# Performance work log

Hardware: AMD Instinct MI355X
Metric: run time of the kernel (lower is better)

## Reference

```python
import jax, jax.numpy as jnp
import numpy as np

U, B, I, D, L = 50000, 20000, 100000, 64, 2
E_UB, E_UI, E_BI = 800000, 1000000, 800000
E_BIAGG, E_UIAGG = 800000, 1000000
UPS_UB = UPS_UI = UPS_BI = 0.1
XI = jnp.array([1.0 / 3, 1.0 / 3, 1.0 / 3], dtype=jnp.float32)  # layer coefs (len L+1)
OMEGA, G1, G2, TAU, LAM1, LAM2 = 0.5, 0.5, 0.5, 0.25, 0.04, 1e-5
BATCH = 2048


def l2norm(x, axis=-1):
    n = jnp.linalg.norm(x, axis=axis, keepdims=True)
    return x / jnp.maximum(n, 1e-12)


def spmm(rows, cols, vals, x, n):
    # sparse [n, m] @ dense [m, D] via gather + segment-sum over COO entries
    return jax.ops.segment_sum(vals[:, None] * x[cols], rows, num_segments=n)


def graph_propagate(rows, cols, vals, A, Bf, noise, ups, xi):
    n = A.shape[0] + Bf.shape[0]
    feats = jnp.concatenate([A, Bf], axis=0)
    alls = [feats]
    for l in range(L):
        feats = spmm(rows, cols, vals, feats, n)
        feats = feats + jnp.sign(feats) * l2norm(noise[l]) * ups  # noise injection
        alls.append(l2norm(feats, axis=1))
    out = jnp.sum(jnp.stack(alls, axis=1) * xi[None, :, None], axis=1)  # weighted layer sum [n, D]
    return out[: A.shape[0]], out[A.shape[0] :]


def graph_aggregate(rows, cols, vals, x, noise, ups, n):
    agg = spmm(rows, cols, vals, x, n)
    return agg + jnp.sign(agg) * l2norm(noise) * ups


def cl_loss(pos, aug):
    pos = l2norm(pos, 1)
    aug = l2norm(aug, 1)
    pos_score = jnp.exp(jnp.sum(pos * aug, axis=1) / TAU)
    ttl = jnp.sum(jnp.exp(pos @ aug.T / TAU), axis=1)
    return -jnp.mean(jnp.log(pos_score / ttl))


def dcbr_forward(users_feature, bundles_feature, items_feature,
                 ub_rows, ub_cols, ub_vals, ui_rows, ui_cols, ui_vals,
                 bi_rows, bi_cols, bi_vals, biagg_rows, biagg_cols, biagg_vals,
                 uiagg_rows, uiagg_cols, uiagg_vals,
                 noise_UB, noise_UI, noise_BI, noise_agg_BI, noise_agg_UI,
                 users, bundles):
    UB_u, UB_b = graph_propagate(ub_rows, ub_cols, ub_vals, users_feature, bundles_feature, noise_UB, UPS_UB, XI)
    UI_u, UI_i = graph_propagate(ui_rows, ui_cols, ui_vals, users_feature, items_feature, noise_UI, UPS_UI, XI)
    UI_b = graph_aggregate(biagg_rows, biagg_cols, biagg_vals, UI_i, noise_agg_BI, UPS_BI, B)
    BI_b, BI_i = graph_propagate(bi_rows, bi_cols, bi_vals, bundles_feature, items_feature, noise_BI, UPS_BI, XI)
    BI_u = graph_aggregate(uiagg_rows, uiagg_cols, uiagg_vals, BI_i, noise_agg_UI, UPS_UI, U)
    users_rep = OMEGA * UI_u + (1 - OMEGA) * BI_u
    bundles_rep = OMEGA * UI_b + (1 - OMEGA) * BI_b
    u_emb = users_rep[users]          # [batch, 1, D] -> broadcasts over negatives
    b_emb = bundles_rep[bundles]      # [batch, 2, D]
    pred = jnp.sum(u_emb * b_emb, axis=2)  # [batch, 2]
    pos, neg = pred[:, :1], pred[:, 1:]
    reg = jnp.sum(users_feature ** 2) + jnp.sum(bundles_feature ** 2) + jnp.sum(items_feature ** 2)
    bpr = -jnp.mean(jax.nn.log_sigmoid(pos - neg)) + LAM2 * reg
    u0, b0 = users[:, 0], bundles[:, 0]
    ub_u, ui_us, bi_us = UB_u[u0], UI_u[u0], BI_u[u0]
    ub_bb, ui_bb, bi_bb = UB_b[b0], UI_b[b0], BI_b[b0]
    u_inter = cl_loss(ub_u, ui_us) + cl_loss(ub_u, bi_us) + cl_loss(ui_us, bi_us)
    b_inter = cl_loss(ub_bb, ui_bb) + cl_loss(ub_bb, bi_bb) + cl_loss(ui_bb, bi_bb)
    u_intra = cl_loss(ub_u, ub_u) + cl_loss(ui_us, ui_us) + cl_loss(bi_us, bi_us)
    b_intra = cl_loss(ub_bb, ub_bb) + cl_loss(ui_bb, ui_bb) + cl_loss(bi_bb, bi_bb)
    cl = LAM1 * (G1 * (u_inter + b_inter) + G2 * (u_intra + b_intra))
    return bpr, cl


def setup_inputs():
    key = jax.random.key(0)
    k = jax.random.split(key, 16)

    def prop_edges(kk, nA, nB, e):
        k1, k2, k3 = jax.random.split(kk, 3)
        a = jax.random.randint(k1, (e,), 0, nA, dtype=jnp.int32)
        b = jax.random.randint(k2, (e,), 0, nB, dtype=jnp.int32) + nA
        v = jax.random.uniform(k3, (e,), jnp.float32, 0.01, 0.2)  # degree-normalized weights
        return jnp.concatenate([a, b]), jnp.concatenate([b, a]), jnp.concatenate([v, v])

    def agg_edges(kk, nA, nB, e):
        k1, k2, k3 = jax.random.split(kk, 3)
        return (jax.random.randint(k1, (e,), 0, nA, dtype=jnp.int32),
                jax.random.randint(k2, (e,), 0, nB, dtype=jnp.int32),
                jax.random.uniform(k3, (e,), jnp.float32, 0.01, 0.2))

    ub_rows, ub_cols, ub_vals = prop_edges(k[0], U, B, E_UB)
    ui_rows, ui_cols, ui_vals = prop_edges(k[1], U, I, E_UI)
    bi_rows, bi_cols, bi_vals = prop_edges(k[2], B, I, E_BI)
    biagg_rows, biagg_cols, biagg_vals = agg_edges(k[3], B, I, E_BIAGG)
    uiagg_rows, uiagg_cols, uiagg_vals = agg_edges(k[4], U, I, E_UIAGG)
    s = 0.02  # xavier-normal-ish scale
    return {
        'users_feature': jax.random.normal(k[5], (U, D), jnp.float32) * s,
        'bundles_feature': jax.random.normal(k[6], (B, D), jnp.float32) * s,
        'items_feature': jax.random.normal(k[7], (I, D), jnp.float32) * s,
        'ub_rows': ub_rows, 'ub_cols': ub_cols, 'ub_vals': ub_vals,
        'ui_rows': ui_rows, 'ui_cols': ui_cols, 'ui_vals': ui_vals,
        'bi_rows': bi_rows, 'bi_cols': bi_cols, 'bi_vals': bi_vals,
        'biagg_rows': biagg_rows, 'biagg_cols': biagg_cols, 'biagg_vals': biagg_vals,
        'uiagg_rows': uiagg_rows, 'uiagg_cols': uiagg_cols, 'uiagg_vals': uiagg_vals,
        'noise_UB': jax.random.uniform(k[8], (L, U + B, D), jnp.float32),
        'noise_UI': jax.random.uniform(k[9], (L, U + I, D), jnp.float32),
        'noise_BI': jax.random.uniform(k[10], (L, B + I, D), jnp.float32),
        'noise_agg_BI': jax.random.uniform(k[11], (B, D), jnp.float32),
        'noise_agg_UI': jax.random.uniform(k[12], (U, D), jnp.float32),
        'users': jax.random.randint(k[13], (BATCH, 1), 0, U, dtype=jnp.int32),
        'bundles': jax.random.randint(k[14], (BATCH, 2), 0, B, dtype=jnp.int32),
    }


def reference(users_feature, bundles_feature, items_feature,
              ub_rows, ub_cols, ub_vals, ui_rows, ui_cols, ui_vals,
              bi_rows, bi_cols, bi_vals, biagg_rows, biagg_cols, biagg_vals,
              uiagg_rows, uiagg_cols, uiagg_vals,
              noise_UB, noise_UI, noise_BI, noise_agg_BI, noise_agg_UI,
              users, bundles):
    return dcbr_forward(users_feature, bundles_feature, items_feature,
                        ub_rows, ub_cols, ub_vals, ui_rows, ui_cols, ui_vals,
                        bi_rows, bi_cols, bi_vals, biagg_rows, biagg_cols, biagg_vals,
                        uiagg_rows, uiagg_cols, uiagg_vals,
                        noise_UB, noise_UI, noise_BI, noise_agg_BI, noise_agg_UI,
                        users, bundles)
```

## Files before the change

kernel.cpp:

```cpp
#include <hip/hip_runtime.h>
#include <cmath>
#include <climits>

#define DD 64

namespace {

constexpr int U_N = 50000, B_N = 20000, I_N = 100000;
constexpr int BATCH = 2048;

constexpr int N1 = 340000, N2 = 70000;
constexpr int SHIFT1 = 10, SHIFT2 = 8;
constexpr int NB1 = (N1 + (1 << SHIFT1) - 1) >> SHIFT1;
constexpr int NB2 = (N2 + (1 << SHIFT2) - 1) >> SHIFT2;

typedef __attribute__((ext_vector_type(8))) short short8;
typedef __attribute__((ext_vector_type(4))) float floatx4;

__device__ __forceinline__ float wave_sum(float v) {
#pragma unroll
  for (int off = 32; off > 0; off >>= 1) v += __shfl_xor(v, off);
  return v;
}

__device__ __forceinline__ unsigned short f2bf(float f) {
  unsigned u = __float_as_uint(f);
  unsigned r = (u + 0x7FFFu + ((u >> 16) & 1u)) >> 16;
  return (unsigned short)r;
}

__device__ __forceinline__ float sgn(float x) {
  return (x > 0.f) ? 1.f : ((x < 0.f) ? -1.f : 0.f);
}

__global__ void k_tobf16(const float* __restrict__ x, unsigned short* __restrict__ o, int n4) {
  int i = blockIdx.x * 256 + threadIdx.x;
  if (i >= n4) return;
  float4 v = ((const float4*)x)[i];
  uint2 p;
  p.x = (unsigned)f2bf(v.x) | ((unsigned)f2bf(v.y) << 16);
  p.y = (unsigned)f2bf(v.z) | ((unsigned)f2bf(v.w) << 16);
  ((uint2*)o)[i] = p;
}

__global__ __launch_bounds__(512) void k_bhist(const int* __restrict__ rows, int nnz,
                                               int row_off, int shift,
                                               const unsigned char* __restrict__ flags,
                                               int* __restrict__ bcnt) {
  __shared__ int h[512];
  int t = threadIdx.x;
  h[t] = 0;
  __syncthreads();
  int tile0 = blockIdx.x * 8192;
#pragma unroll
  for (int i = 0; i < 16; ++i) {
    int e = tile0 + i * 512 + t;
    if (e < nnz) {
      int r = rows[e] + row_off;
      if (!flags || flags[r]) atomicAdd(&h[r >> shift], 1);
    }
  }
  __syncthreads();
  if (h[t]) atomicAdd(&bcnt[t], h[t]);
}

__global__ void k_bucket_scan(const int* __restrict__ bcnt, int nb, int* __restrict__ bbase,
                              int* __restrict__ bcur, int* __restrict__ rowptr_end) {
  int t = threadIdx.x;
  int lane = t & 63, w = t >> 6;
  int v = (t < nb) ? bcnt[t] : 0;
  int inc = v;
#pragma unroll
  for (int off = 1; off < 64; off <<= 1) {
    int y = __shfl_up(inc, off);
    if (lane >= off) inc += y;
  }
  __shared__ int wsum[8];
  if (lane == 63) wsum[w] = inc;
  __syncthreads();
  int wadd = 0;
  for (int i = 0; i < w; ++i) wadd += wsum[i];
  inc += wadd;
  if (t < nb) { bbase[t] = inc - v; bcur[t] = inc - v; }
  if (t == 511) { bbase[nb] = inc; *rowptr_end = inc; }
}

__global__ __launch_bounds__(512) void k_binscatter(const int* __restrict__ rows,
                                                    const int* __restrict__ cols,
                                                    const float* __restrict__ vals, int nnz,
                                                    int row_off, int shift,
                                                    int nAth, int offA, int offB,
                                                    const unsigned char* __restrict__ flags,
                                                    int* __restrict__ bcur,
                                                    int2* __restrict__ ebin_cv) {
  __shared__ int cnt[512];
  __shared__ int gbase[512];
  int t = threadIdx.x;
  int tile0 = blockIdx.x * 8192;
  cnt[t] = 0;
  __syncthreads();
  int r[16], rank[16];
#pragma unroll
  for (int i = 0; i < 16; ++i) {
    int e = tile0 + i * 512 + t;
    rank[i] = -1;
    if (e < nnz) {
      r[i] = rows[e] + row_off;
      if (!flags || flags[r[i]]) rank[i] = atomicAdd(&cnt[r[i] >> shift], 1);
    }
  }
  __syncthreads();
  int c = cnt[t];
  if (c > 0) gbase[t] = atomicAdd(&bcur[t], c);
  __syncthreads();
  int mask = (1 << shift) - 1;
#pragma unroll
  for (int i = 0; i < 16; ++i) {
    int e = tile0 + i * 512 + t;
    if (rank[i] >= 0) {
      int pos = gbase[r[i] >> shift] + rank[i];
      int col = cols[e];
      int gcol = (col < nAth) ? col + offA : col + offB;
      ebin_cv[pos] = make_int2(((r[i] & mask) << 20) | gcol, __float_as_int(vals[e]));
    }
  }
}

__global__ __launch_bounds__(1024) void k_place(const int* __restrict__ bbase, int shift,
                                                int nrows, const int2* __restrict__ ebin_cv,
                                                int* __restrict__ rowptr,
                                                int2* __restrict__ epack) {
  int b = blockIdx.x;
  int bsize = 1 << shift;
  int row0 = b << shift;
  int t = threadIdx.x;
  __shared__ int rcnt[1024];
  __shared__ int wsum[16];
  int ebase = bbase[b], eend = bbase[b + 1];
  if (t < bsize) rcnt[t] = 0;
  __syncthreads();
  for (int e = ebase + t; e < eend; e += 1024)
    atomicAdd(&rcnt[ebin_cv[e].x >> 20], 1);
  __syncthreads();
  int v = (t < bsize) ? rcnt[t] : 0;
  int inc = v;
  int lane = t & 63, w = t >> 6;
#pragma unroll
  for (int off = 1; off < 64; off <<= 1) {
    int y = __shfl_up(inc, off);
    if (lane >= off) inc += y;
  }
  if (lane == 63) wsum[w] = inc;
  __syncthreads();
  int wadd = 0;
  for (int i = 0; i < w; ++i) wadd += wsum[i];
  inc += wadd;
  int excl = inc - v;
  int nr = nrows - row0;
  if (nr > bsize) nr = bsize;
  if (t < nr) rowptr[row0 + t] = ebase + excl;
  __syncthreads();
  if (t < bsize) rcnt[t] = excl;
  __syncthreads();
  for (int e = ebase + t; e < eend; e += 1024) {
    int2 cv = ebin_cv[e];
    int pos = ebase + atomicAdd(&rcnt[cv.x >> 20], 1);
    epack[pos] = make_int2(cv.x & 0xFFFFF, cv.y);
  }
}

__global__ void k_spmm1(const int* __restrict__ rowptr, const int2* __restrict__ epack,
                        const uint2* __restrict__ xg, const float* __restrict__ noise,
                        uint2* __restrict__ s2g, int n, int nAth, int offA, int offB) {
  long long t = (long long)blockIdx.x * 256 + threadIdx.x;
  int row = (int)(t >> 6), lane = (int)(t & 63);
  if (row >= n) return;
  int q = lane >> 4, c = lane & 15;
  int s = rowptr[row], e = rowptr[row + 1];
  float4 a[4];
#pragma unroll
  for (int j = 0; j < 4; ++j) a[j] = (float4){0.f, 0.f, 0.f, 0.f};
  for (int kk = s; kk < e; kk += 16) {
#pragma unroll
    for (int j = 0; j < 4; ++j) {
      int i = kk + 4 * j + q;
      int2 ed = (i < e) ? epack[i] : make_int2(0, 0);
      uint2 d = xg[ed.x * 16 + c];
      float v = __int_as_float(ed.y);
      a[j].x = fmaf(v, __uint_as_float(d.x << 16), a[j].x);
      a[j].y = fmaf(v, __uint_as_float(d.x & 0xffff0000u), a[j].y);
      a[j].z = fmaf(v, __uint_as_float(d.y << 16), a[j].z);
      a[j].w = fmaf(v, __uint_as_float(d.y & 0xffff0000u), a[j].w);
    }
  }
  float4 g;
  g.x = a[0].x + a[1].x + a[2].x + a[3].x;
  g.y = a[0].y + a[1].y + a[2].y + a[3].y;
  g.z = a[0].z + a[1].z + a[2].z + a[3].z;
  g.w = a[0].w + a[1].w + a[2].w + a[3].w;
  g.x += __shfl_xor(g.x, 16); g.y += __shfl_xor(g.y, 16);
  g.z += __shfl_xor(g.z, 16); g.w += __shfl_xor(g.w, 16);
  g.x += __shfl_xor(g.x, 32); g.y += __shfl_xor(g.y, 32);
  g.z += __shfl_xor(g.z, 32); g.w += __shfl_xor(g.w, 32);
  float4 nz = ((const float4*)(noise + (size_t)row * DD))[c];
  float nn = wave_sum(nz.x * nz.x + nz.y * nz.y + nz.z * nz.z + nz.w * nz.w) * 0.25f;
  float nf = 0.1f / fmaxf(sqrtf(nn), 1e-12f);
  if (lane < 16) {
    float4 fv;
    fv.x = g.x + sgn(g.x) * nz.x * nf;
    fv.y = g.y + sgn(g.y) * nz.y * nf;
    fv.z = g.z + sgn(g.z) * nz.z * nf;
    fv.w = g.w + sgn(g.w) * nz.w * nf;
    uint2 o;
    o.x = (unsigned)f2bf(fv.x) | ((unsigned)f2bf(fv.y) << 16);
    o.y = (unsigned)f2bf(fv.z) | ((unsigned)f2bf(fv.w) << 16);
    int grow = (row < nAth) ? row + offA : row + offB;
    s2g[grow * 16 + c] = o;
  }
}

__global__ void k_spmm2(const int* __restrict__ rowptr, const int2* __restrict__ epack,
                        const uint2* __restrict__ s2g, const uint2* __restrict__ xg,
                        const float* __restrict__ noise, float* __restrict__ outp,
                        int n, int nAth, int offA, int offB) {
  long long t = (long long)blockIdx.x * 256 + threadIdx.x;
  int row = (int)(t >> 6), lane = (int)(t & 63);
  if (row >= n) return;
  int q = lane >> 4, c = lane & 15;
  int s = rowptr[row], e = rowptr[row + 1];
  float4 a[4];
#pragma unroll
  for (int j = 0; j < 4; ++j) a[j] = (float4){0.f, 0.f, 0.f, 0.f};
  for (int kk = s; kk < e; kk += 16) {
#pragma unroll
    for (int j = 0; j < 4; ++j) {
      int i = kk + 4 * j + q;
      int2 ed = (i < e) ? epack[i] : make_int2(0, 0);
      uint2 d = s2g[ed.x * 16 + c];
      float v = __int_as_float(ed.y);
      a[j].x = fmaf(v, __uint_as_float(d.x << 16), a[j].x);
      a[j].y = fmaf(v, __uint_as_float(d.x & 0xffff0000u), a[j].y);
      a[j].z = fmaf(v, __uint_as_float(d.y << 16), a[j].z);
      a[j].w = fmaf(v, __uint_as_float(d.y & 0xffff0000u), a[j].w);
    }
  }
  float4 g;
  g.x = a[0].x + a[1].x + a[2].x + a[3].x;
  g.y = a[0].y + a[1].y + a[2].y + a[3].y;
  g.z = a[0].z + a[1].z + a[2].z + a[3].z;
  g.w = a[0].w + a[1].w + a[2].w + a[3].w;
  g.x += __shfl_xor(g.x, 16); g.y += __shfl_xor(g.y, 16);
  g.z += __shfl_xor(g.z, 16); g.w += __shfl_xor(g.w, 16);
  g.x += __shfl_xor(g.x, 32); g.y += __shfl_xor(g.y, 32);
  g.z += __shfl_xor(g.z, 32); g.w += __shfl_xor(g.w, 32);
  float4 nz = ((const float4*)(noise + (size_t)row * DD))[c];
  float nn = wave_sum(nz.x * nz.x + nz.y * nz.y + nz.z * nz.z + nz.w * nz.w) * 0.25f;
  float nf = 0.1f / fmaxf(sqrtf(nn), 1e-12f);
  float4 fv;
  fv.x = g.x + sgn(g.x) * nz.x * nf;
  fv.y = g.y + sgn(g.y) * nz.y * nf;
  fv.z = g.z + sgn(g.z) * nz.z * nf;
  fv.w = g.w + sgn(g.w) * nz.w * nf;
  float fn2 = wave_sum(fv.x * fv.x + fv.y * fv.y + fv.z * fv.z + fv.w * fv.w) * 0.25f;
  float inv2 = (1.f / 3.f) / fmaxf(sqrtf(fn2), 1e-12f);
  int grow = (row < nAth) ? row + offA : row + offB;
  uint2 s1p = s2g[grow * 16 + c];
  float4 s1;
  s1.x = __uint_as_float(s1p.x << 16);
  s1.y = __uint_as_float(s1p.x & 0xffff0000u);
  s1.z = __uint_as_float(s1p.y << 16);
  s1.w = __uint_as_float(s1p.y & 0xffff0000u);
  float fn1 = wave_sum(s1.x * s1.x + s1.y * s1.y + s1.z * s1.z + s1.w * s1.w) * 0.25f;
  float inv1 = (1.f / 3.f) / fmaxf(sqrtf(fn1), 1e-12f);
  uint2 x0p = xg[grow * 16 + c];
  float4 x0;
  x0.x = __uint_as_float(x0p.x << 16);
  x0.y = __uint_as_float(x0p.x & 0xffff0000u);
  x0.z = __uint_as_float(x0p.y << 16);
  x0.w = __uint_as_float(x0p.y & 0xffff0000u);
  if (lane < 16) {
    float4 o;
    o.x = x0.x * (1.f / 3.f) + s1.x * inv1 + fv.x * inv2;
    o.y = x0.y * (1.f / 3.f) + s1.y * inv1 + fv.y * inv2;
    o.z = x0.z * (1.f / 3.f) + s1.z * inv1 + fv.z * inv2;
    o.w = x0.w * (1.f / 3.f) + s1.w * inv1 + fv.w * inv2;
    ((float4*)(outp + (size_t)row * DD))[c] = o;
  }
}

__global__ void k_agg_s(const int* __restrict__ rowptr, const int2* __restrict__ epack,
                        const float* __restrict__ x, const float* __restrict__ noise,
                        const int* __restrict__ ids, int nids, float* __restrict__ out) {
  long long t = (long long)blockIdx.x * 256 + threadIdx.x;
  int w = (int)(t >> 6), lane = (int)(t & 63);
  if (w >= nids) return;
  int row = ids[w];
  int q = lane >> 4, c = lane & 15;
  int s = rowptr[row], e = rowptr[row + 1];
  float4 a0 = {0.f, 0.f, 0.f, 0.f}, a1 = {0.f, 0.f, 0.f, 0.f};
  for (int kk = s; kk < e; kk += 8) {
    int i0 = kk + q, i1 = kk + 4 + q;
    int2 e0 = (i0 < e) ? epack[i0] : make_int2(0, 0);
    int2 e1 = (i1 < e) ? epack[i1] : make_int2(0, 0);
    float4 x0 = ((const float4*)(x + (size_t)e0.x * DD))[c];
    float4 x1 = ((const float4*)(x + (size_t)e1.x * DD))[c];
    float v0 = __int_as_float(e0.y), v1 = __int_as_float(e1.y);
    a0.x = fmaf(v0, x0.x, a0.x); a0.y = fmaf(v0, x0.y, a0.y);
    a0.z = fmaf(v0, x0.z, a0.z); a0.w = fmaf(v0, x0.w, a0.w);
    a1.x = fmaf(v1, x1.x, a1.x); a1.y = fmaf(v1, x1.y, a1.y);
    a1.z = fmaf(v1, x1.z, a1.z); a1.w = fmaf(v1, x1.w, a1.w);
  }
  float4 g;
  g.x = a0.x + a1.x; g.y = a0.y + a1.y; g.z = a0.z + a1.z; g.w = a0.w + a1.w;
  g.x += __shfl_xor(g.x, 16); g.y += __shfl_xor(g.y, 16);
  g.z += __shfl_xor(g.z, 16); g.w += __shfl_xor(g.w, 16);
  g.x += __shfl_xor(g.x, 32); g.y += __shfl_xor(g.y, 32);
  g.z += __shfl_xor(g.z, 32); g.w += __shfl_xor(g.w, 32);
  float4 nz = ((const float4*)(noise + (size_t)row * DD))[c];
  float nn = wave_sum(nz.x * nz.x + nz.y * nz.y + nz.z * nz.z + nz.w * nz.w) * 0.25f;
  float nf = 0.1f / fmaxf(sqrtf(nn), 1e-12f);
  if (lane < 16) {
    float4 fv;
    fv.x = g.x + sgn(g.x) * nz.x * nf;
    fv.y = g.y + sgn(g.y) * nz.y * nf;
    fv.z = g.z + sgn(g.z) * nz.z * nf;
    fv.w = g.w + sgn(g.w) * nz.w * nf;
    ((float4*)(out + (size_t)w * DD))[c] = fv;
  }
}

__global__ void k_flag(const int* __restrict__ users, const int* __restrict__ bundles,
                       unsigned char* __restrict__ flags) {
  int t = blockIdx.x * 256 + threadIdx.x;
  if (t < BATCH) flags[20000 + users[t]] = 1;
  if (t < 2 * BATCH) flags[bundles[t]] = 1;
}


__global__ void k_bpr(const float* __restrict__ o_UI, const float* __restrict__ biuS,
                      const float* __restrict__ uibS, const float* __restrict__ o_BI,
                      const int* __restrict__ users, const int* __restrict__ bundles,
                      float* __restrict__ bpr_terms) {
  long long t = (long long)blockIdx.x * 256 + threadIdx.x;
  int w = (int)(t >> 6);
  int lane = (int)(t & 63);
  if (w >= BATCH) return;
  int u = users[w];
  int b0 = bundles[2 * w], b1 = bundles[2 * w + 1];
  float ur = 0.5f * (o_UI[(size_t)u * DD + lane] + biuS[(size_t)w * DD + lane]);
  float br0 = 0.5f * (uibS[(size_t)(2 * w) * DD + lane] + o_BI[(size_t)b0 * DD + lane]);
  float br1 = 0.5f * (uibS[(size_t)(2 * w + 1) * DD + lane] + o_BI[(size_t)b1 * DD + lane]);
  float pos = wave_sum(ur * br0);
  float neg = wave_sum(ur * br1);
  if (lane == 0) {
    float x = pos - neg;
    float loss = (x > 0.f) ? log1pf(expf(-x)) : (-x + log1pf(expf(x)));
    bpr_terms[w] = loss;
  }
}

__global__ void k_sumsq_p(const float* __restrict__ x, int n4, float* __restrict__ partials) {
  float s = 0.f;
  for (int i = blockIdx.x * 256 + threadIdx.x; i < n4; i += gridDim.x * 256) {
    float4 v = ((const float4*)x)[i];
    s += v.x * v.x + v.y * v.y + v.z * v.z + v.w * v.w;
  }
  s = wave_sum(s);
  __shared__ float part[4];
  if ((threadIdx.x & 63) == 0) part[threadIdx.x >> 6] = s;
  __syncthreads();
  if (threadIdx.x == 0) partials[blockIdx.x] = part[0] + part[1] + part[2] + part[3];
}

__global__ void k_gather(const float* __restrict__ o_UB, const float* __restrict__ o_UI,
                         const float* __restrict__ o_BI, const float* __restrict__ uibS,
                         const float* __restrict__ biuS, const int* __restrict__ users,
                         const int* __restrict__ bundles, float* __restrict__ P,
                         unsigned short* __restrict__ Pb) {
  long long t = (long long)blockIdx.x * 256 + threadIdx.x;
  int w = (int)(t >> 6);
  int lane = (int)(t & 63);
  if (w >= 6 * BATCH) return;
  int k = w / BATCH, b = w % BATCH;
  const float* src;
  if (k == 0)      src = o_UB + (size_t)users[b] * DD;
  else if (k == 1) src = o_UI + (size_t)users[b] * DD;
  else if (k == 2) src = biuS + (size_t)b * DD;
  else if (k == 3) src = o_UB + (size_t)(U_N + bundles[2 * b]) * DD;
  else if (k == 4) src = uibS + (size_t)(2 * b) * DD;
  else             src = o_BI + (size_t)bundles[2 * b] * DD;
  float v = src[lane];
  float n2 = wave_sum(v * v);
  float inv = 1.f / fmaxf(sqrtf(n2), 1e-12f);
  float pv = v * inv;
  P[(size_t)w * DD + lane] = pv;
  Pb[(size_t)w * DD + lane] = f2bf(pv);
}

__global__ void k_clpair_mfma(const unsigned short* __restrict__ Pb,
                              float* __restrict__ ttl) {
  const int pairX[12] = {0, 0, 1, 0, 1, 2, 3, 3, 4, 3, 4, 5};
  const int pairY[12] = {1, 2, 2, 0, 1, 2, 4, 5, 5, 3, 4, 5};
  int wid = threadIdx.x >> 6;
  int lane = threadIdx.x & 63;
  int wtile = blockIdx.x * 4 + wid;
  int p = wtile >> 8;
  int rest = wtile & 255;
  int it = rest >> 3, jc = rest & 7;
  const unsigned short* X = Pb + (size_t)pairX[p] * BATCH * DD;
  const unsigned short* Y = Pb + (size_t)pairY[p] * BATCH * DD;
  int r = lane & 15, q = lane >> 4;
  short8 A[2][4];
#pragma unroll
  for (int kh = 0; kh < 2; ++kh)
#pragma unroll
    for (int ii = 0; ii < 4; ++ii)
      A[kh][ii] = *(const short8*)(X + (size_t)(it * 64 + ii * 16 + r) * DD + kh * 32 + q * 8);
  float rs[4][4];
#pragma unroll
  for (int ii = 0; ii < 4; ++ii)
#pragma unroll
    for (int g = 0; g < 4; ++g) rs[ii][g] = 0.f;
  for (int jn = 0; jn < 4; ++jn) {
    int j0 = jc * 256 + jn * 64;
    floatx4 acc[4][4];
#pragma unroll
    for (int ii = 0; ii < 4; ++ii)
#pragma unroll
      for (int jj = 0; jj < 4; ++jj) acc[ii][jj] = (floatx4){0.f, 0.f, 0.f, 0.f};
#pragma unroll
    for (int kh = 0; kh < 2; ++kh) {
      short8 Bf[4];
#pragma unroll
      for (int jj = 0; jj < 4; ++jj)
        Bf[jj] = *(const short8*)(Y + (size_t)(j0 + jj * 16 + r) * DD + kh * 32 + q * 8);
#pragma unroll
      for (int ii = 0; ii < 4; ++ii)
#pragma unroll
        for (int jj = 0; jj < 4; ++jj)
          acc[ii][jj] = __builtin_amdgcn_mfma_f32_16x16x32_bf16(A[kh][ii], Bf[jj],
                                                                acc[ii][jj], 0, 0, 0);
    }
#pragma unroll
    for (int ii = 0; ii < 4; ++ii)
#pragma unroll
      for (int jj = 0; jj < 4; ++jj)
#pragma unroll
        for (int g = 0; g < 4; ++g) rs[ii][g] += __expf(4.0f * acc[ii][jj][g]);
  }
#pragma unroll
  for (int off = 1; off < 16; off <<= 1)
#pragma unroll
    for (int ii = 0; ii < 4; ++ii)
#pragma unroll
      for (int g = 0; g < 4; ++g) rs[ii][g] += __shfl_xor(rs[ii][g], off);
  if (r == 0) {
#pragma unroll
    for (int ii = 0; ii < 4; ++ii)
#pragma unroll
      for (int g = 0; g < 4; ++g)
        unsafeAtomicAdd(&ttl[(size_t)p * BATCH + it * 64 + ii * 16 + q * 4 + g],
                        rs[ii][g]);
  }
}

__global__ void k_cldiag(const float* __restrict__ P, float* __restrict__ ttl) {
  const int pairX[12] = {0, 0, 1, 0, 1, 2, 3, 3, 4, 3, 4, 5};
  const int pairY[12] = {1, 2, 2, 0, 1, 2, 4, 5, 5, 3, 4, 5};
  long long t = (long long)blockIdx.x * 256 + threadIdx.x;
  int w = (int)(t >> 6);
  int lane = (int)(t & 63);
  if (w >= 12 * BATCH) return;
  int p = w / BATCH, i = w % BATCH;
  float xv = P[((size_t)pairX[p] * BATCH + i) * DD + lane];
  float yv = P[((size_t)pairY[p] * BATCH + i) * DD + lane];
  float d = wave_sum(xv * yv);
  if (lane == 0) ttl[(size_t)p * BATCH + i] = logf(ttl[(size_t)p * BATCH + i]) - d * 4.0f;
}

__global__ void k_finalred(const float* __restrict__ bpr_terms,
                           const float* __restrict__ cl_terms,
                           const float* __restrict__ partials,
                           float* __restrict__ out) {
  int t = threadIdx.x;
  float bpr = 0.f, reg = 0.f, inter = 0.f, intra = 0.f;
  for (int i = t; i < BATCH; i += 1024) bpr += bpr_terms[i];
  for (int i = t; i < 768; i += 1024) reg += partials[i];
  for (int i = t; i < 12 * BATCH; i += 1024) {
    int p = i >> 11;
    float v = cl_terms[i];
    if ((p % 6) < 3) inter += v; else intra += v;
  }
  bpr = wave_sum(bpr); reg = wave_sum(reg);
  inter = wave_sum(inter); intra = wave_sum(intra);
  __shared__ float sb[16], sr[16], si[16], sx[16];
  int w = t >> 6, lane = t & 63;
  if (lane == 0) { sb[w] = bpr; sr[w] = reg; si[w] = inter; sx[w] = intra; }
  __syncthreads();
  if (t == 0) {
    float Bs = 0, Rs = 0, Is = 0, Xs = 0;
    for (int i = 0; i < 16; ++i) { Bs += sb[i]; Rs += sr[i]; Is += si[i]; Xs += sx[i]; }
    out[0] = Bs / (float)BATCH + 1e-5f * Rs;
    out[1] = 0.04f * (0.5f * Is + 0.5f * Xs) / (float)BATCH;
  }
}

}

extern "C" void kernel_launch(void* const* d_in, const int* in_sizes, int n_in,
                              void* d_out, int out_size, void* d_ws, size_t ws_size,
                              hipStream_t stream) {
  const float* usersF = (const float*)d_in[0];
  const float* bundlesF = (const float*)d_in[1];
  const float* itemsF = (const float*)d_in[2];
  const int* ub_rows = (const int*)d_in[3];
  const int* ub_cols = (const int*)d_in[4];
  const float* ub_vals = (const float*)d_in[5];
  const int* ui_rows = (const int*)d_in[6];
  const int* ui_cols = (const int*)d_in[7];
  const float* ui_vals = (const float*)d_in[8];
  const int* bi_rows = (const int*)d_in[9];
  const int* bi_cols = (const int*)d_in[10];
  const float* bi_vals = (const float*)d_in[11];
  const int* biagg_rows = (const int*)d_in[12];
  const int* biagg_cols = (const int*)d_in[13];
  const float* biagg_vals = (const float*)d_in[14];
  const int* uiagg_rows = (const int*)d_in[15];
  const int* uiagg_cols = (const int*)d_in[16];
  const float* uiagg_vals = (const float*)d_in[17];
  const float* noise_UB = (const float*)d_in[18];
  const float* noise_UI = (const float*)d_in[19];
  const float* noise_BI = (const float*)d_in[20];
  const float* noise_agg_BI = (const float*)d_in[21];
  const float* noise_agg_UI = (const float*)d_in[22];
  const int* users = (const int*)d_in[23];
  const int* bundles = (const int*)d_in[24];
  int nnz_ub = in_sizes[3], nnz_ui = in_sizes[6], nnz_bi = in_sizes[9];
  int nnz_biagg = in_sizes[12], nnz_uiagg = in_sizes[15];

  float* ws = (float*)d_ws;
  size_t off = 0;
  float* o_UB = ws + off; off += (size_t)(U_N + B_N) * DD;
  float* o_UI = ws + off; off += (size_t)(U_N + I_N) * DD;
  float* o_BI = ws + off; off += (size_t)(B_N + I_N) * DD;
  float* uibS = ws + off; off += (size_t)2 * BATCH * DD;
  float* biuS = ws + off; off += (size_t)BATCH * DD;
  unsigned short* s2g16 = (unsigned short*)(ws + off); off += (size_t)170000 * DD / 2;
  unsigned short* xb16  = (unsigned short*)(ws + off); off += (size_t)170000 * DD / 2;
  float* P    = ws + off; off += (size_t)6 * BATCH * DD;
  float* ttl  = ws + off; off += (size_t)12 * BATCH;
  float* bprT = ws + off; off += BATCH;
  float* prt  = ws + off; off += 768;
  int* rptr  = (int*)(ws + off); off += N1 + 1;
  int* bcnt  = (int*)(ws + off); off += 512;
  int* bbase = (int*)(ws + off); off += 520;
  int* bcur  = (int*)(ws + off); off += 512;
  unsigned char* flags = (unsigned char*)(ws + off); off += 17500;
  off = (off + 1) & ~(size_t)1;
  int2* epack = (int2*)(ws + off); off += (size_t)5200000 * 2;
  if (ws_size < off * sizeof(float)) return;

  unsigned short* Pb = (unsigned short*)s2g16;
  int2* ebin_cv1 = (int2*)ws;
  int2* ebin_cv2 = (int2*)s2g16;

  const uint2* xgv = (const uint2*)xb16;
  uint2* s2gv = (uint2*)s2g16;

  auto gb = [](int nnz) { return (nnz + 8191) / 8192; };

  k_tobf16<<<(U_N * 16 + 255) / 256, 256, 0, stream>>>(usersF, xb16, U_N * 16);
  k_tobf16<<<(B_N * 16 + 255) / 256, 256, 0, stream>>>(bundlesF, xb16 + (size_t)U_N * DD,
                                                       B_N * 16);
  k_tobf16<<<(I_N * 16 + 255) / 256, 256, 0, stream>>>(itemsF, xb16 + (size_t)(U_N + B_N) * DD,
                                                       I_N * 16);

  int* rp_ub = rptr, * rp_ui = rptr + 70000, * rp_bi = rptr + 220000;
  hipMemsetAsync(bcnt, 0, 512 * sizeof(int), stream);
  k_bhist<<<gb(nnz_ub), 512, 0, stream>>>(ub_rows, nnz_ub, 0, SHIFT1, nullptr, bcnt);
  k_bhist<<<gb(nnz_ui), 512, 0, stream>>>(ui_rows, nnz_ui, 70000, SHIFT1, nullptr, bcnt);
  k_bhist<<<gb(nnz_bi), 512, 0, stream>>>(bi_rows, nnz_bi, 220000, SHIFT1, nullptr, bcnt);
  k_bucket_scan<<<1, 512, 0, stream>>>(bcnt, NB1, bbase, bcur, rptr + N1);
  k_binscatter<<<gb(nnz_ub), 512, 0, stream>>>(ub_rows, ub_cols, ub_vals, nnz_ub, 0, SHIFT1,
                                               INT_MAX, 0, 0, nullptr, bcur, ebin_cv1);
  k_binscatter<<<gb(nnz_ui), 512, 0, stream>>>(ui_rows, ui_cols, ui_vals, nnz_ui, 70000, SHIFT1,
                                               50000, 0, 20000, nullptr, bcur, ebin_cv1);
  k_binscatter<<<gb(nnz_bi), 512, 0, stream>>>(bi_rows, bi_cols, bi_vals, nnz_bi, 220000, SHIFT1,
                                               0, 50000, 50000, nullptr, bcur, ebin_cv1);
  k_place<<<NB1, 1024, 0, stream>>>(bbase, SHIFT1, N1, ebin_cv1, rptr, epack);

  auto propagate = [&](int nA, int nB, const int* rp, const float* noise, float* outp,
                       int nAth, int offA, int offB) {
    int n = nA + nB;
    int gp = (int)(((long long)n * 64 + 255) / 256);
    k_spmm1<<<gp, 256, 0, stream>>>(rp, epack, xgv, noise, s2gv, n, nAth, offA, offB);
    k_spmm2<<<gp, 256, 0, stream>>>(rp, epack, s2gv, xgv, noise + (size_t)n * DD,
                                    outp, n, nAth, offA, offB);
  };

  propagate(U_N, B_N, rp_ub, noise_UB, o_UB, INT_MAX, 0, 0);
  propagate(U_N, I_N, rp_ui, noise_UI, o_UI, 50000, 0, 20000);
  propagate(B_N, I_N, rp_bi, noise_BI, o_BI, 0, 50000, 50000);

  int* rp_ba = rptr, * rp_ua = rptr + 20000;
  hipMemsetAsync(flags, 0, 70000, stream);
  k_flag<<<(2 * BATCH + 255) / 256, 256, 0, stream>>>(users, bundles, flags);
  hipMemsetAsync(bcnt, 0, 512 * sizeof(int), stream);
  k_bhist<<<gb(nnz_biagg), 512, 0, stream>>>(biagg_rows, nnz_biagg, 0, SHIFT2, flags, bcnt);
  k_bhist<<<gb(nnz_uiagg), 512, 0, stream>>>(uiagg_rows, nnz_uiagg, 20000, SHIFT2, flags, bcnt);
  k_bucket_scan<<<1, 512, 0, stream>>>(bcnt, NB2, bbase, bcur, rptr + N2);
  k_binscatter<<<gb(nnz_biagg), 512, 0, stream>>>(biagg_rows, biagg_cols, biagg_vals, nnz_biagg,
                                                  0, SHIFT2, INT_MAX, 0, 0, flags, bcur,
                                                  ebin_cv2);
  k_binscatter<<<gb(nnz_uiagg), 512, 0, stream>>>(uiagg_rows, uiagg_cols, uiagg_vals, nnz_uiagg,
                                                  20000, SHIFT2, INT_MAX, 0, 0, flags, bcur,
                                                  ebin_cv2);
  k_place<<<NB2, 1024, 0, stream>>>(bbase, SHIFT2, N2, ebin_cv2, rptr, epack);

  k_agg_s<<<(2 * BATCH * 64) / 256, 256, 0, stream>>>(
      rp_ba, epack, o_UI + (size_t)U_N * DD, noise_agg_BI, bundles, 2 * BATCH, uibS);
  k_agg_s<<<(BATCH * 64) / 256, 256, 0, stream>>>(
      rp_ua, epack, o_BI + (size_t)B_N * DD, noise_agg_UI, users, BATCH, biuS);

  k_bpr<<<BATCH * 64 / 256, 256, 0, stream>>>(o_UI, biuS, uibS, o_BI, users, bundles, bprT);
  k_sumsq_p<<<256, 256, 0, stream>>>(usersF, U_N * DD / 4, prt);
  k_sumsq_p<<<256, 256, 0, stream>>>(bundlesF, B_N * DD / 4, prt + 256);
  k_sumsq_p<<<256, 256, 0, stream>>>(itemsF, I_N * DD / 4, prt + 512);
  k_gather<<<6 * BATCH * 64 / 256, 256, 0, stream>>>(o_UB, o_UI, o_BI, uibS, biuS,
                                                     users, bundles, P, Pb);
  hipMemsetAsync(ttl, 0, (size_t)12 * BATCH * sizeof(float), stream);
  k_clpair_mfma<<<768, 256, 0, stream>>>(Pb, ttl);
  k_cldiag<<<12 * BATCH * 64 / 256, 256, 0, stream>>>(P, ttl);
  k_finalred<<<1, 1024, 0, stream>>>(bprT, ttl, prt, (float*)d_out);
}
```

Measured before the change: 1.065 ms.

## Compute second propagation layer only for batch-referenced rows and aggregated items

The second SpMM layer of each graph propagation now runs only for rows the loss actually reads: the batch users and bundles through an index list, plus all items that feed the later aggregation. Outputs are written compactly per batch slot, and the BPR and gather kernels read them directly instead of indexing by id. The inner SpMM loops also switch to clamped edge loads with packed two-wide FMAs, and norm reductions use a 16-lane shuffle instead of the full wave. This drops the second layer for most user and bundle rows, at the cost of extra launches and duplicate work when batch ids repeat.

```diff
diff --git a/kernel.cpp b/kernel.cpp
--- a/kernel.cpp
+++ b/kernel.cpp
@@ -16,10 +16,17 @@
 
 typedef __attribute__((ext_vector_type(8))) short short8;
 typedef __attribute__((ext_vector_type(4))) float floatx4;
+typedef __attribute__((ext_vector_type(2))) float f32x2;
 
 __device__ __forceinline__ float wave_sum(float v) {
 #pragma unroll
   for (int off = 32; off > 0; off >>= 1) v += __shfl_xor(v, off);
+  return v;
+}
+
+__device__ __forceinline__ float wave_sum16(float v) {
+#pragma unroll
+  for (int off = 1; off < 16; off <<= 1) v += __shfl_xor(v, off);
   return v;
 }
 
@@ -176,34 +183,36 @@
   int row = (int)(t >> 6), lane = (int)(t & 63);
   if (row >= n) return;
   int q = lane >> 4, c = lane & 15;
+  unsigned cb = (unsigned)c << 3;
   int s = rowptr[row], e = rowptr[row + 1];
-  float4 a[4];
-#pragma unroll
-  for (int j = 0; j < 4; ++j) a[j] = (float4){0.f, 0.f, 0.f, 0.f};
+  int em1 = e - 1;
+  f32x2 a0[4], a1[4];
+#pragma unroll
+  for (int j = 0; j < 4; ++j) { a0[j] = (f32x2){0.f, 0.f}; a1[j] = (f32x2){0.f, 0.f}; }
   for (int kk = s; kk < e; kk += 16) {
 #pragma unroll
     for (int j = 0; j < 4; ++j) {
       int i = kk + 4 * j + q;
-      int2 ed = (i < e) ? epack[i] : make_int2(0, 0);
-      uint2 d = xg[ed.x * 16 + c];
-      float v = __int_as_float(ed.y);
-      a[j].x = fmaf(v, __uint_as_float(d.x << 16), a[j].x);
-      a[j].y = fmaf(v, __uint_as_float(d.x & 0xffff0000u), a[j].y);
-      a[j].z = fmaf(v, __uint_as_float(d.y << 16), a[j].z);
-      a[j].w = fmaf(v, __uint_as_float(d.y & 0xffff0000u), a[j].w);
+      int ic = min(i, em1);
+      int2 ed = epack[ic];
+      float v = (i <= em1) ? __int_as_float(ed.y) : 0.f;
+      uint2 d = *(const uint2*)((const char*)xg + (((unsigned)ed.x << 7) | cb));
+      f32x2 lo = {__uint_as_float(d.x << 16), __uint_as_float(d.x & 0xffff0000u)};
+      f32x2 hi = {__uint_as_float(d.y << 16), __uint_as_float(d.y & 0xffff0000u)};
+      f32x2 vv = {v, v};
+      a0[j] = __builtin_elementwise_fma(lo, vv, a0[j]);
+      a1[j] = __builtin_elementwise_fma(hi, vv, a1[j]);
     }
   }
-  float4 g;
-  g.x = a[0].x + a[1].x + a[2].x + a[3].x;
-  g.y = a[0].y + a[1].y + a[2].y + a[3].y;
-  g.z = a[0].z + a[1].z + a[2].z + a[3].z;
-  g.w = a[0].w + a[1].w + a[2].w + a[3].w;
+  f32x2 g0 = (a0[0] + a0[1]) + (a0[2] + a0[3]);
+  f32x2 g1 = (a1[0] + a1[1]) + (a1[2] + a1[3]);
+  float4 g = {g0.x, g0.y, g1.x, g1.y};
   g.x += __shfl_xor(g.x, 16); g.y += __shfl_xor(g.y, 16);
   g.z += __shfl_xor(g.z, 16); g.w += __shfl_xor(g.w, 16);
   g.x += __shfl_xor(g.x, 32); g.y += __shfl_xor(g.y, 32);
   g.z += __shfl_xor(g.z, 32); g.w += __shfl_xor(g.w, 32);
   float4 nz = ((const float4*)(noise + (size_t)row * DD))[c];
-  float nn = wave_sum(nz.x * nz.x + nz.y * nz.y + nz.z * nz.z + nz.w * nz.w) * 0.25f;
+  float nn = wave_sum16(nz.x * nz.x + nz.y * nz.y + nz.z * nz.z + nz.w * nz.w) * 0.25f;
   float nf = 0.1f / fmaxf(sqrtf(nn), 1e-12f);
   if (lane < 16) {
     float4 fv;
@@ -222,46 +231,50 @@
 __global__ void k_spmm2(const int* __restrict__ rowptr, const int2* __restrict__ epack,
                         const uint2* __restrict__ s2g, const uint2* __restrict__ xg,
                         const float* __restrict__ noise, float* __restrict__ outp,
-                        int n, int nAth, int offA, int offB) {
+                        const int* __restrict__ ids, int row_add, int row0, int nw,
+                        int nAth, int offA, int offB) {
   long long t = (long long)blockIdx.x * 256 + threadIdx.x;
-  int row = (int)(t >> 6), lane = (int)(t & 63);
-  if (row >= n) return;
+  int w = (int)(t >> 6), lane = (int)(t & 63);
+  if (w >= nw) return;
+  int row = ids ? (ids[w] + row_add) : (row0 + w);
   int q = lane >> 4, c = lane & 15;
+  unsigned cb = (unsigned)c << 3;
   int s = rowptr[row], e = rowptr[row + 1];
-  float4 a[4];
-#pragma unroll
-  for (int j = 0; j < 4; ++j) a[j] = (float4){0.f, 0.f, 0.f, 0.f};
+  int em1 = e - 1;
+  f32x2 a0[4], a1[4];
+#pragma unroll
+  for (int j = 0; j < 4; ++j) { a0[j] = (f32x2){0.f, 0.f}; a1[j] = (f32x2){0.f, 0.f}; }
   for (int kk = s; kk < e; kk += 16) {
 #pragma unroll
     for (int j = 0; j < 4; ++j) {
       int i = kk + 4 * j + q;
-      int2 ed = (i < e) ? epack[i] : make_int2(0, 0);
-      uint2 d = s2g[ed.x * 16 + c];
-      float v = __int_as_float(ed.y);
-      a[j].x = fmaf(v, __uint_as_float(d.x << 16), a[j].x);
-      a[j].y = fmaf(v, __uint_as_float(d.x & 0xffff0000u), a[j].y);
-      a[j].z = fmaf(v, __uint_as_float(d.y << 16), a[j].z);
-      a[j].w = fmaf(v, __uint_as_float(d.y & 0xffff0000u), a[j].w);
+      int ic = min(i, em1);
+      int2 ed = epack[ic];
+      float v = (i <= em1) ? __int_as_float(ed.y) : 0.f;
+      uint2 d = *(const uint2*)((const char*)s2g + (((unsigned)ed.x << 7) | cb));
+      f32x2 lo = {__uint_as_float(d.x << 16), __uint_as_float(d.x & 0xffff0000u)};
+      f32x2 hi = {__uint_as_float(d.y << 16), __uint_as_float(d.y & 0xffff0000u)};
+      f32x2 vv = {v, v};
+      a0[j] = __builtin_elementwise_fma(lo, vv, a0[j]);
+      a1[j] = __builtin_elementwise_fma(hi, vv, a1[j]);
     }
   }
-  float4 g;
-  g.x = a[0].x + a[1].x + a[2].x + a[3].x;
-  g.y = a[0].y + a[1].y + a[2].y + a[3].y;
-  g.z = a[0].z + a[1].z + a[2].z + a[3].z;
-  g.w = a[0].w + a[1].w + a[2].w + a[3].w;
+  f32x2 g0 = (a0[0] + a0[1]) + (a0[2] + a0[3]);
+  f32x2 g1 = (a1[0] + a1[1]) + (a1[2] + a1[3]);
+  float4 g = {g0.x, g0.y, g1.x, g1.y};
   g.x += __shfl_xor(g.x, 16); g.y += __shfl_xor(g.y, 16);
   g.z += __shfl_xor(g.z, 16); g.w += __shfl_xor(g.w, 16);
   g.x += __shfl_xor(g.x, 32); g.y += __shfl_xor(g.y, 32);
   g.z += __shfl_xor(g.z, 32); g.w += __shfl_xor(g.w, 32);
   float4 nz = ((const float4*)(noise + (size_t)row * DD))[c];
-  float nn = wave_sum(nz.x * nz.x + nz.y * nz.y + nz.z * nz.z + nz.w * nz.w) * 0.25f;
+  float nn = wave_sum16(nz.x * nz.x + nz.y * nz.y + nz.z * nz.z + nz.w * nz.w) * 0.25f;
   float nf = 0.1f / fmaxf(sqrtf(nn), 1e-12f);
   float4 fv;
   fv.x = g.x + sgn(g.x) * nz.x * nf;
   fv.y = g.y + sgn(g.y) * nz.y * nf;
   fv.z = g.z + sgn(g.z) * nz.z * nf;
   fv.w = g.w + sgn(g.w) * nz.w * nf;
-  float fn2 = wave_sum(fv.x * fv.x + fv.y * fv.y + fv.z * fv.z + fv.w * fv.w) * 0.25f;
+  float fn2 = wave_sum16(fv.x * fv.x + fv.y * fv.y + fv.z * fv.z + fv.w * fv.w) * 0.25f;
   float inv2 = (1.f / 3.f) / fmaxf(sqrtf(fn2), 1e-12f);
   int grow = (row < nAth) ? row + offA : row + offB;
   uint2 s1p = s2g[grow * 16 + c];
@@ -270,7 +283,7 @@
   s1.y = __uint_as_float(s1p.x & 0xffff0000u);
   s1.z = __uint_as_float(s1p.y << 16);
   s1.w = __uint_as_float(s1p.y & 0xffff0000u);
-  float fn1 = wave_sum(s1.x * s1.x + s1.y * s1.y + s1.z * s1.z + s1.w * s1.w) * 0.25f;
+  float fn1 = wave_sum16(s1.x * s1.x + s1.y * s1.y + s1.z * s1.z + s1.w * s1.w) * 0.25f;
   float inv1 = (1.f / 3.f) / fmaxf(sqrtf(fn1), 1e-12f);
   uint2 x0p = xg[grow * 16 + c];
   float4 x0;
@@ -284,7 +297,7 @@
     o.y = x0.y * (1.f / 3.f) + s1.y * inv1 + fv.y * inv2;
     o.z = x0.z * (1.f / 3.f) + s1.z * inv1 + fv.z * inv2;
     o.w = x0.w * (1.f / 3.f) + s1.w * inv1 + fv.w * inv2;
-    ((float4*)(outp + (size_t)row * DD))[c] = o;
+    ((float4*)(outp + (size_t)w * DD))[c] = o;
   }
 }
 
@@ -297,14 +310,16 @@
   int row = ids[w];
   int q = lane >> 4, c = lane & 15;
   int s = rowptr[row], e = rowptr[row + 1];
+  int em1 = e - 1;
   float4 a0 = {0.f, 0.f, 0.f, 0.f}, a1 = {0.f, 0.f, 0.f, 0.f};
   for (int kk = s; kk < e; kk += 8) {
     int i0 = kk + q, i1 = kk + 4 + q;
-    int2 e0 = (i0 < e) ? epack[i0] : make_int2(0, 0);
-    int2 e1 = (i1 < e) ? epack[i1] : make_int2(0, 0);
+    int2 e0 = epack[min(i0, em1)];
+    int2 e1 = epack[min(i1, em1)];
     float4 x0 = ((const float4*)(x + (size_t)e0.x * DD))[c];
     float4 x1 = ((const float4*)(x + (size_t)e1.x * DD))[c];
-    float v0 = __int_as_float(e0.y), v1 = __int_as_float(e1.y);
+    float v0 = (i0 <= em1) ? __int_as_float(e0.y) : 0.f;
+    float v1 = (i1 <= em1) ? __int_as_float(e1.y) : 0.f;
     a0.x = fmaf(v0, x0.x, a0.x); a0.y = fmaf(v0, x0.y, a0.y);
     a0.z = fmaf(v0, x0.z, a0.z); a0.w = fmaf(v0, x0.w, a0.w);
     a1.x = fmaf(v1, x1.x, a1.x); a1.y = fmaf(v1, x1.y, a1.y);
@@ -317,7 +332,7 @@
   g.x += __shfl_xor(g.x, 32); g.y += __shfl_xor(g.y, 32);
   g.z += __shfl_xor(g.z, 32); g.w += __shfl_xor(g.w, 32);
   float4 nz = ((const float4*)(noise + (size_t)row * DD))[c];
-  float nn = wave_sum(nz.x * nz.x + nz.y * nz.y + nz.z * nz.z + nz.w * nz.w) * 0.25f;
+  float nn = wave_sum16(nz.x * nz.x + nz.y * nz.y + nz.z * nz.z + nz.w * nz.w) * 0.25f;
   float nf = 0.1f / fmaxf(sqrtf(nn), 1e-12f);
   if (lane < 16) {
     float4 fv;
@@ -336,20 +351,17 @@
   if (t < 2 * BATCH) flags[bundles[t]] = 1;
 }
 
-
-__global__ void k_bpr(const float* __restrict__ o_UI, const float* __restrict__ biuS,
-                      const float* __restrict__ uibS, const float* __restrict__ o_BI,
-                      const int* __restrict__ users, const int* __restrict__ bundles,
+__global__ void k_bpr(const float* __restrict__ o_UIuS, const float* __restrict__ biuS,
+                      const float* __restrict__ uibS, const float* __restrict__ o_BIbS,
                       float* __restrict__ bpr_terms) {
   long long t = (long long)blockIdx.x * 256 + threadIdx.x;
   int w = (int)(t >> 6);
   int lane = (int)(t & 63);
   if (w >= BATCH) return;
-  int u = users[w];
-  int b0 = bundles[2 * w], b1 = bundles[2 * w + 1];
-  float ur = 0.5f * (o_UI[(size_t)u * DD + lane] + biuS[(size_t)w * DD + lane]);
-  float br0 = 0.5f * (uibS[(size_t)(2 * w) * DD + lane] + o_BI[(size_t)b0 * DD + lane]);
-  float br1 = 0.5f * (uibS[(size_t)(2 * w + 1) * DD + lane] + o_BI[(size_t)b1 * DD + lane]);
+  float ur = 0.5f * (o_UIuS[(size_t)w * DD + lane] + biuS[(size_t)w * DD + lane]);
+  float br0 = 0.5f * (uibS[(size_t)(2 * w) * DD + lane] + o_BIbS[(size_t)(2 * w) * DD + lane]);
+  float br1 = 0.5f * (uibS[(size_t)(2 * w + 1) * DD + lane] +
+                      o_BIbS[(size_t)(2 * w + 1) * DD + lane]);
   float pos = wave_sum(ur * br0);
   float neg = wave_sum(ur * br1);
   if (lane == 0) {
@@ -372,10 +384,9 @@
   if (threadIdx.x == 0) partials[blockIdx.x] = part[0] + part[1] + part[2] + part[3];
 }
 
-__global__ void k_gather(const float* __restrict__ o_UB, const float* __restrict__ o_UI,
-                         const float* __restrict__ o_BI, const float* __restrict__ uibS,
-                         const float* __restrict__ biuS, const int* __restrict__ users,
-                         const int* __restrict__ bundles, float* __restrict__ P,
+__global__ void k_gather(const float* __restrict__ o_UBS, const float* __restrict__ o_UIuS,
+                         const float* __restrict__ o_BIbS, const float* __restrict__ uibS,
+                         const float* __restrict__ biuS, float* __restrict__ P,
                          unsigned short* __restrict__ Pb) {
   long long t = (long long)blockIdx.x * 256 + threadIdx.x;
   int w = (int)(t >> 6);
@@ -383,12 +394,12 @@
   if (w >= 6 * BATCH) return;
   int k = w / BATCH, b = w % BATCH;
   const float* src;
-  if (k == 0)      src = o_UB + (size_t)users[b] * DD;
-  else if (k == 1) src = o_UI + (size_t)users[b] * DD;
+  if (k == 0)      src = o_UBS + (size_t)b * DD;
+  else if (k == 1) src = o_UIuS + (size_t)b * DD;
   else if (k == 2) src = biuS + (size_t)b * DD;
-  else if (k == 3) src = o_UB + (size_t)(U_N + bundles[2 * b]) * DD;
+  else if (k == 3) src = o_UBS + (size_t)(2048 + 2 * b) * DD;
   else if (k == 4) src = uibS + (size_t)(2 * b) * DD;
-  else             src = o_BI + (size_t)bundles[2 * b] * DD;
+  else             src = o_BIbS + (size_t)(2 * b) * DD;
   float v = src[lane];
   float n2 = wave_sum(v * v);
   float inv = 1.f / fmaxf(sqrtf(n2), 1e-12f);
@@ -540,9 +551,11 @@
 
   float* ws = (float*)d_ws;
   size_t off = 0;
-  float* o_UB = ws + off; off += (size_t)(U_N + B_N) * DD;
-  float* o_UI = ws + off; off += (size_t)(U_N + I_N) * DD;
-  float* o_BI = ws + off; off += (size_t)(B_N + I_N) * DD;
+  float* o_UBS  = ws + off; off += (size_t)(3 * BATCH) * DD;
+  float* o_UIuS = ws + off; off += (size_t)BATCH * DD;
+  float* o_UIit = ws + off; off += (size_t)I_N * DD;
+  float* o_BIbS = ws + off; off += (size_t)(2 * BATCH) * DD;
+  float* o_BIit = ws + off; off += (size_t)I_N * DD;
   float* uibS = ws + off; off += (size_t)2 * BATCH * DD;
   float* biuS = ws + off; off += (size_t)BATCH * DD;
   unsigned short* s2g16 = (unsigned short*)(ws + off); off += (size_t)170000 * DD / 2;
@@ -589,18 +602,39 @@
                                                0, 50000, 50000, nullptr, bcur, ebin_cv1);
   k_place<<<NB1, 1024, 0, stream>>>(bbase, SHIFT1, N1, ebin_cv1, rptr, epack);
 
-  auto propagate = [&](int nA, int nB, const int* rp, const float* noise, float* outp,
-                       int nAth, int offA, int offB) {
-    int n = nA + nB;
-    int gp = (int)(((long long)n * 64 + 255) / 256);
-    k_spmm1<<<gp, 256, 0, stream>>>(rp, epack, xgv, noise, s2gv, n, nAth, offA, offB);
-    k_spmm2<<<gp, 256, 0, stream>>>(rp, epack, s2gv, xgv, noise + (size_t)n * DD,
-                                    outp, n, nAth, offA, offB);
-  };
-
-  propagate(U_N, B_N, rp_ub, noise_UB, o_UB, INT_MAX, 0, 0);
-  propagate(U_N, I_N, rp_ui, noise_UI, o_UI, 50000, 0, 20000);
-  propagate(B_N, I_N, rp_bi, noise_BI, o_BI, 0, 50000, 50000);
+  {
+    int n = 70000;
+    k_spmm1<<<(int)(((long long)n * 64 + 255) / 256), 256, 0, stream>>>(
+        rp_ub, epack, xgv, noise_UB, s2gv, n, INT_MAX, 0, 0);
+    const float* nz2 = noise_UB + (size_t)n * DD;
+    k_spmm2<<<BATCH * 64 / 256, 256, 0, stream>>>(rp_ub, epack, s2gv, xgv, nz2, o_UBS,
+                                                  users, 0, 0, BATCH, INT_MAX, 0, 0);
+    k_spmm2<<<2 * BATCH * 64 / 256, 256, 0, stream>>>(rp_ub, epack, s2gv, xgv, nz2,
+                                                      o_UBS + (size_t)2048 * DD,
+                                                      bundles, 50000, 0, 2 * BATCH,
+                                                      INT_MAX, 0, 0);
+  }
+  {
+    int n = 150000;
+    k_spmm1<<<(int)(((long long)n * 64 + 255) / 256), 256, 0, stream>>>(
+        rp_ui, epack, xgv, noise_UI, s2gv, n, 50000, 0, 20000);
+    const float* nz2 = noise_UI + (size_t)n * DD;
+    k_spmm2<<<BATCH * 64 / 256, 256, 0, stream>>>(rp_ui, epack, s2gv, xgv, nz2, o_UIuS,
+                                                  users, 0, 0, BATCH, 50000, 0, 20000);
+    k_spmm2<<<(int)(((long long)I_N * 64 + 255) / 256), 256, 0, stream>>>(
+        rp_ui, epack, s2gv, xgv, nz2, o_UIit, nullptr, 0, 50000, I_N, 50000, 0, 20000);
+  }
+  {
+    int n = 120000;
+    k_spmm1<<<(int)(((long long)n * 64 + 255) / 256), 256, 0, stream>>>(
+        rp_bi, epack, xgv, noise_BI, s2gv, n, 0, 50000, 50000);
+    const float* nz2 = noise_BI + (size_t)n * DD;
+    k_spmm2<<<2 * BATCH * 64 / 256, 256, 0, stream>>>(rp_bi, epack, s2gv, xgv, nz2, o_BIbS,
+                                                      bundles, 0, 0, 2 * BATCH, 0, 50000,
+                                                      50000);
+    k_spmm2<<<(int)(((long long)I_N * 64 + 255) / 256), 256, 0, stream>>>(
+        rp_bi, epack, s2gv, xgv, nz2, o_BIit, nullptr, 0, 20000, I_N, 0, 50000, 50000);
+  }
 
   int* rp_ba = rptr, * rp_ua = rptr + 20000;
   hipMemsetAsync(flags, 0, 70000, stream);
@@ -618,16 +652,16 @@
   k_place<<<NB2, 1024, 0, stream>>>(bbase, SHIFT2, N2, ebin_cv2, rptr, epack);
 
   k_agg_s<<<(2 * BATCH * 64) / 256, 256, 0, stream>>>(
-      rp_ba, epack, o_UI + (size_t)U_N * DD, noise_agg_BI, bundles, 2 * BATCH, uibS);
+      rp_ba, epack, o_UIit, noise_agg_BI, bundles, 2 * BATCH, uibS);
   k_agg_s<<<(BATCH * 64) / 256, 256, 0, stream>>>(
-      rp_ua, epack, o_BI + (size_t)B_N * DD, noise_agg_UI, users, BATCH, biuS);
-
-  k_bpr<<<BATCH * 64 / 256, 256, 0, stream>>>(o_UI, biuS, uibS, o_BI, users, bundles, bprT);
+      rp_ua, epack, o_BIit, noise_agg_UI, users, BATCH, biuS);
+
+  k_bpr<<<BATCH * 64 / 256, 256, 0, stream>>>(o_UIuS, biuS, uibS, o_BIbS, bprT);
   k_sumsq_p<<<256, 256, 0, stream>>>(usersF, U_N * DD / 4, prt);
   k_sumsq_p<<<256, 256, 0, stream>>>(bundlesF, B_N * DD / 4, prt + 256);
   k_sumsq_p<<<256, 256, 0, stream>>>(itemsF, I_N * DD / 4, prt + 512);
-  k_gather<<<6 * BATCH * 64 / 256, 256, 0, stream>>>(o_UB, o_UI, o_BI, uibS, biuS,
-                                                     users, bundles, P, Pb);
+  k_gather<<<6 * BATCH * 64 / 256, 256, 0, stream>>>(o_UBS, o_UIuS, o_BIbS, uibS, biuS,
+                                                     P, Pb);
   hipMemsetAsync(ttl, 0, (size_t)12 * BATCH * sizeof(float), stream);
   k_clpair_mfma<<<768, 256, 0, stream>>>(Pb, ttl);
   k_cldiag<<<12 * BATCH * 64 / 256, 256, 0, stream>>>(P, ttl);
```

New measurement: 998.1 us. 6.3% less time.
